# Kernel tuning notes

Measured on AMD Instinct MI355X. Metric: run time of the kernel, lower is better.

## Reference

```python
import jax, jax.numpy as jnp
import numpy as np

B, S, D, H = 4, 2048, 1024, 16
HD = D // H  # head_dim = 64


def setup_inputs() -> dict:
    key = jax.random.key(0)
    ks = jax.random.split(key, 7)
    sc = 0.02
    return {
        "data": jax.random.normal(ks[0], (B, S, D), jnp.float32),
        "context": jax.random.normal(ks[1], (B, S, D), jnp.float32),
        "Wq": jax.random.normal(ks[2], (D, D), jnp.float32) * sc,
        "bq": jnp.zeros((D,), jnp.float32),
        "Wk": jax.random.normal(ks[3], (D, D), jnp.float32) * sc,
        "bk": jnp.zeros((D,), jnp.float32),
        "Wv": jax.random.normal(ks[4], (D, D), jnp.float32) * sc,
        "bv": jnp.zeros((D,), jnp.float32),
        "Wo": jax.random.normal(ks[5], (D, D), jnp.float32) * sc,
        "bo": jnp.zeros((D,), jnp.float32),
    }


def reference(data, context, Wq, bq, Wk, bk, Wv, bv, Wo, bo):
    # Projections (torch Linear: x @ W.T + b; here W stored as [in, out])
    Q = data @ Wq + bq          # [B,S,D]
    K = context @ Wk + bk
    V = context @ Wv + bv
    # split heads -> [B,H,S,HD]
    Q = Q.reshape(B, S, H, HD).transpose(0, 2, 1, 3)
    K = K.reshape(B, S, H, HD).transpose(0, 2, 1, 3)
    V = V.reshape(B, S, H, HD).transpose(0, 2, 1, 3)
    scale = jnp.sqrt(jnp.asarray(HD, Q.dtype))
    scores = jnp.einsum("bhqd,bhkd->bhqk", Q, K) / scale  # [B,H,S,S]
    causal = jnp.tril(jnp.ones((S, S), bool))              # row >= col
    scores = jnp.where(causal[None, None], scores, jnp.asarray(-jnp.inf, scores.dtype))
    probs = jax.nn.softmax(scores, axis=-1)
    Z = jnp.einsum("bhqk,bhkd->bhqd", probs, V)            # [B,H,S,HD]
    Z = Z.transpose(0, 2, 1, 3).reshape(B, S, D)
    return Z @ Wo + bo
```

## Files before the change

kernel.cpp:

```cpp
#include <hip/hip_runtime.h>

#define B_  4
#define S_  2048
#define D_  1024
#define H_  16
#define HD_ 64
#define M_  (B_*S_)

typedef _Float16 f16;
typedef f16  f16x8 __attribute__((ext_vector_type(8)));
typedef f16  f16x4 __attribute__((ext_vector_type(4)));
typedef float f32x4 __attribute__((ext_vector_type(4)));

__device__ __forceinline__ void gload_lds16(const f16* g, f16* l) {
    __builtin_amdgcn_global_load_lds(
        (const __attribute__((address_space(1))) void*)g,
        (__attribute__((address_space(3))) void*)l, 16, 0, 0);
}

__global__ __launch_bounds__(256) void cvt2_kernel(const float* __restrict__ a,
                                                   const float* __restrict__ c,
                                                   f16* __restrict__ out, int n4each) {
    int i = blockIdx.x * 256 + threadIdx.x;
    const float* src = (i < n4each) ? a : c;
    int j = (i < n4each) ? i : i - n4each;
    f32x4 v = *reinterpret_cast<const f32x4*>(src + (size_t)j * 4);
    *reinterpret_cast<f16x4*>(out + (size_t)i * 4) = __builtin_convertvector(v, f16x4);
}

__global__ __launch_bounds__(256) void transpose_cvt4_kernel(const float* __restrict__ Wq,
                                                             const float* __restrict__ Wk,
                                                             const float* __restrict__ Wv,
                                                             const float* __restrict__ Wo,
                                                             f16* __restrict__ WT) {
    __shared__ float tile[32][33];
    const int z = blockIdx.z;
    const float* W = (z == 0) ? Wq : (z == 1) ? Wk : (z == 2) ? Wv : Wo;
    f16* dst = WT + (size_t)z * D_ * D_;
    const int n0 = blockIdx.x * 32, k0 = blockIdx.y * 32;
    const int tx = threadIdx.x & 31, ty = threadIdx.x >> 5;
#pragma unroll
    for (int j = 0; j < 4; ++j)
        tile[ty + 8 * j][tx] = W[(size_t)(k0 + ty + 8 * j) * D_ + n0 + tx];
    __syncthreads();
#pragma unroll
    for (int j = 0; j < 4; ++j)
        dst[(size_t)(n0 + ty + 8 * j) * D_ + k0 + tx] = (f16)tile[tx][ty + 8 * j];
}

__global__ __launch_bounds__(512, 2) void gemm_qkv8(const f16* __restrict__ Adata,
                                                    const f16* __restrict__ Actx,
                                                    const f16* __restrict__ Wt,
                                                    const float* __restrict__ bq,
                                                    const float* __restrict__ bk,
                                                    const float* __restrict__ bv,
                                                    f16* __restrict__ Qb,
                                                    f16* __restrict__ Kb,
                                                    f16* __restrict__ VtB) {
    extern __shared__ __align__(16) f16 SM[];
    constexpr int K = D_;
    constexpr int NT = K / 64;
    const int id = (int)(blockIdx.y * 12 + blockIdx.x);
    const int work = (id & 7) * 48 + (id >> 3);
    const int wy = work / 12, wx = work - wy * 12;
    const int seg = wx >> 2;
    const f16* __restrict__ A = seg ? Actx : Adata;
    const int m0 = wy * 256, n0 = wx * 256;
    const int tid = (int)threadIdx.x;
    const int w = tid >> 6, l = tid & 63, lr = l & 15, lg = l >> 4;
    const int wr = w >> 2, wc = w & 3;
    const int swx = lr & 7;
    const int srow = tid >> 3;
    const int g16 = (tid & 7) ^ (srow & 7);

    auto stageH = [&](int buf, int kt, int mat, int h) {
        const f16* __restrict__ src = mat ? (Wt + (size_t)(n0 + h * 128) * K)
                                          : (A + (size_t)(m0 + h * 128) * K);
        f16* dst = SM + mat * 32768 + buf * 16384 + h * 8192;
        const int kk0 = kt * 64;
        gload_lds16(src + (size_t)srow * K + kk0 + g16 * 8, dst + w * 512);
        gload_lds16(src + (size_t)(srow + 64) * K + kk0 + g16 * 8, dst + 4096 + w * 512);
    };
    auto LDA = [&](int buf, int m, int kk) -> f16x8 {
        const int gr = m * 32 + wr * 16 + lr;
        return *reinterpret_cast<const f16x8*>(
            SM + buf * 16384 + (gr >> 7) * 8192 + (gr & 127) * 64 + (((kk * 4 + lg) ^ swx) * 8));
    };
    auto LDB = [&](int buf, int n, int kk) -> f16x8 {
        const int gr = n * 64 + wc * 16 + lr;
        return *reinterpret_cast<const f16x8*>(
            SM + 32768 + buf * 16384 + (gr >> 7) * 8192 + (gr & 127) * 64 + (((kk * 4 + lg) ^ swx) * 8));
    };

    f32x4 acc[8][4] = {};
    stageH(0, 0, 0, 0); stageH(0, 0, 1, 0); stageH(0, 0, 1, 1); stageH(0, 0, 0, 1);
    asm volatile("s_waitcnt vmcnt(4)" ::: "memory");
    __builtin_amdgcn_s_barrier();

    for (int t = 0; t < NT; ++t) {
        const int buf = t & 1, nb = buf ^ 1;
        const bool nl = (t + 1 < NT);
        f16x8 a[4][2], b[4][2];
#pragma unroll
        for (int m = 0; m < 4; ++m) { a[m][0] = LDA(buf, m, 0); a[m][1] = LDA(buf, m, 1); }
#pragma unroll
        for (int n = 0; n < 2; ++n) { b[n][0] = LDB(buf, n, 0); b[n][1] = LDB(buf, n, 1); }
        if (nl) { stageH(nb, t + 1, 0, 0); asm volatile("s_waitcnt vmcnt(4)" ::: "memory"); }
        else    { asm volatile("s_waitcnt vmcnt(2)" ::: "memory"); }
        __builtin_amdgcn_s_barrier();
        __builtin_amdgcn_s_setprio(1);
#pragma unroll
        for (int kk = 0; kk < 2; ++kk)
#pragma unroll
            for (int m = 0; m < 4; ++m)
#pragma unroll
                for (int n = 0; n < 2; ++n)
                    acc[m][n] = __builtin_amdgcn_mfma_f32_16x16x32_f16(a[m][kk], b[n][kk], acc[m][n], 0, 0, 0);
        __builtin_amdgcn_s_setprio(0);
        __builtin_amdgcn_s_barrier();
#pragma unroll
        for (int n = 2; n < 4; ++n) { b[n][0] = LDB(buf, n, 0); b[n][1] = LDB(buf, n, 1); }
        if (nl) { stageH(nb, t + 1, 1, 0); asm volatile("s_waitcnt vmcnt(4)" ::: "memory"); }
        else    { asm volatile("s_waitcnt vmcnt(0)" ::: "memory"); }
        __builtin_amdgcn_s_barrier();
        __builtin_amdgcn_s_setprio(1);
#pragma unroll
        for (int kk = 0; kk < 2; ++kk)
#pragma unroll
            for (int m = 0; m < 4; ++m)
#pragma unroll
                for (int n = 2; n < 4; ++n)
                    acc[m][n] = __builtin_amdgcn_mfma_f32_16x16x32_f16(a[m][kk], b[n][kk], acc[m][n], 0, 0, 0);
        __builtin_amdgcn_s_setprio(0);
        __builtin_amdgcn_s_barrier();
#pragma unroll
        for (int m = 0; m < 4; ++m) { a[m][0] = LDA(buf, m + 4, 0); a[m][1] = LDA(buf, m + 4, 1); }
        if (nl) stageH(nb, t + 1, 1, 1);
        __builtin_amdgcn_s_barrier();
        __builtin_amdgcn_s_setprio(1);
#pragma unroll
        for (int kk = 0; kk < 2; ++kk)
#pragma unroll
            for (int m = 0; m < 4; ++m)
#pragma unroll
                for (int n = 2; n < 4; ++n)
                    acc[m + 4][n] = __builtin_amdgcn_mfma_f32_16x16x32_f16(a[m][kk], b[n][kk], acc[m + 4][n], 0, 0, 0);
        __builtin_amdgcn_s_setprio(0);
        __builtin_amdgcn_s_barrier();
        if (nl) { stageH(nb, t + 1, 0, 1); asm volatile("s_waitcnt vmcnt(4)" ::: "memory"); }
        __builtin_amdgcn_s_barrier();
        __builtin_amdgcn_s_setprio(1);
#pragma unroll
        for (int kk = 0; kk < 2; ++kk)
#pragma unroll
            for (int m = 0; m < 4; ++m)
#pragma unroll
                for (int n = 0; n < 2; ++n)
                    acc[m + 4][n] = __builtin_amdgcn_mfma_f32_16x16x32_f16(a[m][kk], b[n][kk], acc[m + 4][n], 0, 0, 0);
        __builtin_amdgcn_s_setprio(0);
        __builtin_amdgcn_s_barrier();
    }
    const float* bias = (seg == 0) ? bq : (seg == 1) ? bk : bv;
#pragma unroll
    for (int n = 0; n < 4; ++n) {
        const int col = n0 + n * 64 + wc * 16 + lr;
        const int lc = col & 1023;
        const float bvv = bias[lc];
#pragma unroll
        for (int m = 0; m < 8; ++m) {
            const int row = m0 + m * 32 + wr * 16 + lg * 4;
            if (seg == 2) {
                const int bb = row >> 11, s0 = row & 2047;
                f16x4 v;
#pragma unroll
                for (int r = 0; r < 4; ++r) v[r] = (f16)(acc[m][n][r] + bvv);
                *reinterpret_cast<f16x4*>(VtB + ((size_t)(bb * D_ + lc)) * S_ + s0) = v;
            } else {
                f16* dst = seg ? Kb : Qb;
#pragma unroll
                for (int r = 0; r < 4; ++r)
                    dst[(size_t)(row + r) * D_ + lc] = (f16)(acc[m][n][r] + bvv);
            }
        }
    }
}

__global__ __launch_bounds__(256) void gemm_out(const f16* __restrict__ A,
                                                const f16* __restrict__ Bt,
                                                const float* __restrict__ bias,
                                                float* __restrict__ C) {
    constexpr int K = D_;
    constexpr int NT = K / 32;
    __shared__ __align__(16) f16 Al[2][128 * 32];
    __shared__ __align__(16) f16 Bl[2][128 * 32];
    const int id = (int)(blockIdx.y * 8 + blockIdx.x);
    const int work = (id & 7) * 64 + (id >> 3);
    const int wy = work >> 3, wx = work & 7;
    const int m0 = wy * 128, n0 = wx * 128;
    const int tid = threadIdx.x;
    const int w = tid >> 6, l = tid & 63, lr = l & 15, lg = l >> 4;
    const int wr = w >> 1, wc = w & 1;
    const int srow = tid >> 2, soff = (tid & 3) * 8;

    auto stage = [&](int buf, int kk) {
#pragma unroll
        for (int i = 0; i < 2; ++i) {
            const int row = srow + i * 64;
            gload_lds16(A  + (size_t)(m0 + row) * K + kk + soff, &Al[buf][(w + 4 * i) * 512]);
            gload_lds16(Bt + (size_t)(n0 + row) * K + kk + soff, &Bl[buf][(w + 4 * i) * 512]);
        }
    };

    f32x4 acc[4][4] = {};
    stage(0, 0);
    for (int t = 0; t < NT; ++t) {
        const int buf = t & 1;
        if (t + 1 < NT) {
            stage(buf ^ 1, (t + 1) * 32);
            asm volatile("s_waitcnt vmcnt(4)" ::: "memory");
        } else {
            asm volatile("s_waitcnt vmcnt(0)" ::: "memory");
        }
        __builtin_amdgcn_s_barrier();
        f16x8 a[4], b[4];
#pragma unroll
        for (int m = 0; m < 4; ++m)
            a[m] = *reinterpret_cast<const f16x8*>(&Al[buf][(wr * 64 + m * 16 + lr) * 32 + lg * 8]);
#pragma unroll
        for (int n = 0; n < 4; ++n)
            b[n] = *reinterpret_cast<const f16x8*>(&Bl[buf][(wc * 64 + n * 16 + lr) * 32 + lg * 8]);
        __builtin_amdgcn_s_setprio(1);
#pragma unroll
        for (int m = 0; m < 4; ++m)
#pragma unroll
            for (int n = 0; n < 4; ++n)
                acc[m][n] = __builtin_amdgcn_mfma_f32_16x16x32_f16(a[m], b[n], acc[m][n], 0, 0, 0);
        __builtin_amdgcn_s_setprio(0);
        __builtin_amdgcn_s_barrier();
    }
#pragma unroll
    for (int n = 0; n < 4; ++n) {
        const int col = n0 + wc * 64 + n * 16 + lr;
        const float bv = bias[col];
#pragma unroll
        for (int m = 0; m < 4; ++m) {
            const int row = m0 + wr * 64 + m * 16 + lg * 4;
#pragma unroll
            for (int r = 0; r < 4; ++r)
                C[(size_t)(row + r) * D_ + col] = acc[m][n][r] + bv;
        }
    }
}

__global__ __launch_bounds__(256, 2) void attn_kernel(const f16* __restrict__ Q,
                                                      const f16* __restrict__ Kg,
                                                      const f16* __restrict__ Vt,
                                                      f16* __restrict__ Z) {
    __shared__ __align__(16) f16 KL[2][64 * 64];
    __shared__ __align__(16) f16 VL[2][64 * 64];
    __shared__ __align__(16) f16 Pl[4][32][72];
    const int h = blockIdx.x, b = blockIdx.y, pp = blockIdx.z;
    const int tid = threadIdx.x, w = tid >> 6, l = tid & 63, lr = l & 15, lg = l >> 4;
    const size_t base   = ((size_t)b * S_) * D_ + h * HD_;
    const size_t vtbase = ((size_t)(b * D_ + h * HD_)) * S_;
    const f16* __restrict__ Kbase = Kg + base;
    const f16* __restrict__ Vbase = Vt + vtbase;
    const float sc = 0.125f * 1.44269504f;
    const int sw_xor = lr & 7;

    auto stageKV = [&](int buf, int t0) {
#pragma unroll
        for (int i = 0; i < 2; ++i) {
            const int c = i * 256 + tid;
            const int row = c >> 3, g16 = (c & 7) ^ (row & 7);
            f16* dstK = &KL[buf][(i * 256 + w * 64) * 8];
            f16* dstV = &VL[buf][(i * 256 + w * 64) * 8];
            gload_lds16(Kbase + (size_t)(t0 + row) * D_ + g16 * 8, dstK);
            gload_lds16(Vbase + (size_t)row * S_ + t0 + g16 * 8, dstV);
        }
    };

    for (int half = 0; half < 2; ++half) {
        const int qt = half ? pp : (15 - pp);
        const int q0 = qt * 128, wq0 = q0 + w * 32;
        const int ntw = ((wq0 + 31) >> 6) + 1;
        const int ntb = qt * 2 + 2;

        f16x8 qf[2][2];
#pragma unroll
        for (int mf = 0; mf < 2; ++mf)
#pragma unroll
            for (int kd = 0; kd < 2; ++kd)
                qf[mf][kd] = *reinterpret_cast<const f16x8*>(
                    Q + base + (size_t)(wq0 + mf * 16 + lr) * D_ + kd * 32 + lg * 8);

        f32x4 zacc[2][4] = {};
        float mrun[2] = {-3.0e38f, -3.0e38f}, lsum[2] = {0.f, 0.f};

        stageKV(0, 0);
        for (int t = 0; t < ntb; ++t) {
            const int buf = t & 1;
            if (t + 1 < ntb) {
                stageKV(buf ^ 1, (t + 1) * 64);
                asm volatile("s_waitcnt vmcnt(4)" ::: "memory");
            } else {
                asm volatile("s_waitcnt vmcnt(0)" ::: "memory");
            }
            __builtin_amdgcn_s_barrier();
            if (t < ntw) {
                const int t0 = t * 64;
                f16x8 kf[2][4];
#pragma unroll
                for (int kd = 0; kd < 2; ++kd)
#pragma unroll
                    for (int n = 0; n < 4; ++n)
                        kf[kd][n] = *reinterpret_cast<const f16x8*>(
                            &KL[buf][(n * 16 + lr) * 64 + (((kd * 4 + lg) ^ sw_xor) * 8)]);
                f32x4 sf[2][4] = {};
                __builtin_amdgcn_s_setprio(1);
#pragma unroll
                for (int kd = 0; kd < 2; ++kd)
#pragma unroll
                    for (int n = 0; n < 4; ++n)
#pragma unroll
                        for (int mf = 0; mf < 2; ++mf)
                            sf[mf][n] = __builtin_amdgcn_mfma_f32_16x16x32_f16(kf[kd][n], qf[mf][kd], sf[mf][n], 0, 0, 0);
                __builtin_amdgcn_s_setprio(0);
                f16x8 vf[2][4];
#pragma unroll
                for (int kt = 0; kt < 2; ++kt)
#pragma unroll
                    for (int n = 0; n < 4; ++n)
                        vf[kt][n] = *reinterpret_cast<const f16x8*>(
                            &VL[buf][(n * 16 + lr) * 64 + (((kt * 4 + lg) ^ sw_xor) * 8)]);
                if (t == ntw - 1) {
#pragma unroll
                    for (int mf = 0; mf < 2; ++mf)
#pragma unroll
                        for (int n = 0; n < 4; ++n)
#pragma unroll
                            for (int r = 0; r < 4; ++r)
                                if ((t0 + n * 16 + lg * 4 + r) > (wq0 + mf * 16 + lr))
                                    sf[mf][n][r] = -3.0e38f;
                }
#pragma unroll
                for (int mf = 0; mf < 2; ++mf) {
                    f32x4 t4;
#pragma unroll
                    for (int r = 0; r < 4; ++r)
                        t4[r] = fmaxf(fmaxf(sf[mf][0][r], sf[mf][1][r]), fmaxf(sf[mf][2][r], sf[mf][3][r]));
                    float vmax = fmaxf(fmaxf(t4[0], t4[1]), fmaxf(t4[2], t4[3]));
                    vmax = fmaxf(vmax, __shfl_xor(vmax, 16));
                    vmax = fmaxf(vmax, __shfl_xor(vmax, 32));
                    const float vs = vmax * sc;
                    const bool norm = !__all(vs <= mrun[mf] + 10.0f);
                    float al = 1.0f;
                    if (norm) {
                        const float mnew = fmaxf(mrun[mf], vs);
                        al = __builtin_amdgcn_exp2f(mrun[mf] - mnew);
                        mrun[mf] = mnew;
                    }
                    float s = 0.f;
#pragma unroll
                    for (int n = 0; n < 4; ++n) {
                        f32x4 p;
#pragma unroll
                        for (int r = 0; r < 4; ++r)
                            p[r] = __builtin_amdgcn_exp2f(fmaf(sf[mf][n][r], sc, -mrun[mf]));
                        sf[mf][n] = p;
                        s += (p[0] + p[1]) + (p[2] + p[3]);
                    }
                    s += __shfl_xor(s, 16);
                    s += __shfl_xor(s, 32);
#pragma unroll
                    for (int n = 0; n < 4; ++n) {
                        f16x4 pv;
#pragma unroll
                        for (int r = 0; r < 4; ++r) pv[r] = (f16)sf[mf][n][r];
                        *reinterpret_cast<f16x4*>(&Pl[w][mf * 16 + lr][n * 16 + lg * 4]) = pv;
                    }
                    if (norm) {
                        lsum[mf] = lsum[mf] * al + s;
#pragma unroll
                        for (int r = 0; r < 4; ++r) {
                            const float ar = __shfl(al, lg * 4 + r);
#pragma unroll
                            for (int n = 0; n < 4; ++n) zacc[mf][n][r] *= ar;
                        }
                    } else {
                        lsum[mf] += s;
                    }
                }
#pragma unroll
                for (int kt = 0; kt < 2; ++kt) {
                    f16x8 pa[2];
#pragma unroll
                    for (int mf = 0; mf < 2; ++mf)
                        pa[mf] = *reinterpret_cast<const f16x8*>(&Pl[w][mf * 16 + lr][kt * 32 + lg * 8]);
                    __builtin_amdgcn_s_setprio(1);
#pragma unroll
                    for (int n = 0; n < 4; ++n)
#pragma unroll
                        for (int mf = 0; mf < 2; ++mf)
                            zacc[mf][n] = __builtin_amdgcn_mfma_f32_16x16x32_f16(pa[mf], vf[kt][n], zacc[mf][n], 0, 0, 0);
                    __builtin_amdgcn_s_setprio(0);
                }
            }
            __builtin_amdgcn_s_barrier();
        }
#pragma unroll
        for (int mf = 0; mf < 2; ++mf) {
            const float inv = 1.0f / lsum[mf];
#pragma unroll
            for (int r = 0; r < 4; ++r) {
                const float ir = __shfl(inv, lg * 4 + r);
#pragma unroll
                for (int n = 0; n < 4; ++n)
                    Z[base + (size_t)(wq0 + mf * 16 + lg * 4 + r) * D_ + n * 16 + lr] =
                        (f16)(zacc[mf][n][r] * ir);
            }
        }
    }
}

extern "C" void kernel_launch(void* const* d_in, const int* in_sizes, int n_in,
                              void* d_out, int out_size, void* d_ws, size_t ws_size,
                              hipStream_t stream) {
    const float* data    = (const float*)d_in[0];
    const float* context = (const float*)d_in[1];
    const float* Wq = (const float*)d_in[2];
    const float* bq = (const float*)d_in[3];
    const float* Wk = (const float*)d_in[4];
    const float* bk = (const float*)d_in[5];
    const float* Wv = (const float*)d_in[6];
    const float* bv = (const float*)d_in[7];
    const float* Wo = (const float*)d_in[8];
    const float* bo = (const float*)d_in[9];

    const size_t MD = (size_t)M_ * D_;
    const size_t DD = (size_t)D_ * D_;
    f16* dataB = (f16*)d_ws;
    f16* ctxB  = dataB + MD;
    f16* WqT   = ctxB + MD;
    f16* WkT   = WqT + DD;
    f16* WvT   = WkT + DD;
    f16* WoT   = WvT + DD;
    f16* Qb    = WoT + DD;
    f16* Kb    = Qb + MD;
    f16* VtB   = Kb + MD;
    f16* Zb    = VtB + MD;

    (void)WkT; (void)WvT;

    const int n4 = (int)(MD / 4);
    cvt2_kernel<<<2 * n4 / 256, 256, 0, stream>>>(data, context, dataB, n4);
    transpose_cvt4_kernel<<<dim3(32, 32, 4), 256, 0, stream>>>(Wq, Wk, Wv, Wo, WqT);

    static bool attr_set = false;
    if (!attr_set) {
        hipFuncSetAttribute(reinterpret_cast<const void*>(gemm_qkv8),
                            hipFuncAttributeMaxDynamicSharedMemorySize, 131072);
        attr_set = true;
    }
    gemm_qkv8<<<dim3(12, 32), 512, 131072, stream>>>(dataB, ctxB, WqT, bq, bk, bv, Qb, Kb, VtB);

    attn_kernel<<<dim3(H_, B_, 8), 256, 0, stream>>>(Qb, Kb, VtB, Zb);

    gemm_out<<<dim3(8, 64), 256, 0, stream>>>(Zb, WoT, bo, (float*)d_out);
}
```

Measured before the change: 188.2 us.

## Widen output GEMM tile with triple-buffered swizzled LDS; compute softmax row sums via MFMA

The output projection GEMM now uses 128x256 tiles with a three-stage global-to-LDS pipeline, an XOR-swizzled LDS layout and a single barrier per K step. This halves the block count and raises operand reuse per block. In attention, the per-row softmax denominator is accumulated by an extra MFMA of P against a ones vector instead of shuffle reductions, and rescaling is folded into the norm branch. The row sum now comes from f16-rounded probabilities, which slightly changes numerics. The larger accumulator array adds register pressure, and hipFuncSetAttribute is now called on every launch.

Result: faster. 174.7 us (-7.2%).

```diff
diff --git a/kernel.cpp b/kernel.cpp
--- a/kernel.cpp
+++ b/kernel.cpp
@@ -185,69 +185,93 @@
     }
 }
 
-__global__ __launch_bounds__(256) void gemm_out(const f16* __restrict__ A,
-                                                const f16* __restrict__ Bt,
-                                                const float* __restrict__ bias,
-                                                float* __restrict__ C) {
+__global__ __launch_bounds__(256, 2) void gemm_out3(const f16* __restrict__ A,
+                                                    const f16* __restrict__ Wt,
+                                                    const float* __restrict__ bias,
+                                                    float* __restrict__ Cout) {
+    extern __shared__ __align__(16) f16 SM[];
     constexpr int K = D_;
     constexpr int NT = K / 32;
-    __shared__ __align__(16) f16 Al[2][128 * 32];
-    __shared__ __align__(16) f16 Bl[2][128 * 32];
-    const int id = (int)(blockIdx.y * 8 + blockIdx.x);
-    const int work = (id & 7) * 64 + (id >> 3);
-    const int wy = work >> 3, wx = work & 7;
-    const int m0 = wy * 128, n0 = wx * 128;
-    const int tid = threadIdx.x;
-    const int w = tid >> 6, l = tid & 63, lr = l & 15, lg = l >> 4;
+    const int id = (int)blockIdx.x;
+    const int work = (id & 7) * 32 + (id >> 3);
+    const int wy = work >> 2, wx = work & 3;
+    const int m0 = wy * 128, n0 = wx * 256;
+    const int tid = (int)threadIdx.x;
+    const int w = tid >> 6, lr = tid & 15, lg = (tid & 63) >> 4;
     const int wr = w >> 1, wc = w & 1;
-    const int srow = tid >> 2, soff = (tid & 3) * 8;
-
-    auto stage = [&](int buf, int kk) {
-#pragma unroll
-        for (int i = 0; i < 2; ++i) {
-            const int row = srow + i * 64;
-            gload_lds16(A  + (size_t)(m0 + row) * K + kk + soff, &Al[buf][(w + 4 * i) * 512]);
-            gload_lds16(Bt + (size_t)(n0 + row) * K + kk + soff, &Bl[buf][(w + 4 * i) * 512]);
-        }
-    };
-
-    f32x4 acc[4][4] = {};
+    const int sw = (lr >> 1) & 3;
+
+    auto stage = [&](int buf, int kt) {
+        const int kk0 = kt * 32;
+        f16* base = SM + buf * 12288;
+#pragma unroll
+        for (int j = 0; j < 2; ++j) {
+            const int c = j * 256 + tid;
+            const int row = c >> 2;
+            const int ks = ((c & 3) ^ ((row >> 1) & 3)) * 8;
+            gload_lds16(A + (size_t)(m0 + row) * K + kk0 + ks,
+                        base + (j * 256 + w * 64) * 8);
+        }
+#pragma unroll
+        for (int j = 0; j < 4; ++j) {
+            const int c = j * 256 + tid;
+            const int row = c >> 2;
+            const int ks = ((c & 3) ^ ((row >> 1) & 3)) * 8;
+            gload_lds16(Wt + (size_t)(n0 + row) * K + kk0 + ks,
+                        base + 4096 + (j * 256 + w * 64) * 8);
+        }
+    };
+    auto LDA = [&](int buf, int m) -> f16x8 {
+        return *reinterpret_cast<const f16x8*>(
+            SM + buf * 12288 + (wr * 64 + m * 16 + lr) * 32 + ((lg ^ sw) * 8));
+    };
+    auto LDB = [&](int buf, int n) -> f16x8 {
+        return *reinterpret_cast<const f16x8*>(
+            SM + buf * 12288 + 4096 + (wc * 128 + n * 16 + lr) * 32 + ((lg ^ sw) * 8));
+    };
+
+    f32x4 acc[4][8] = {};
     stage(0, 0);
+    stage(1, 1);
+    asm volatile("s_waitcnt vmcnt(6)" ::: "memory");
+    __builtin_amdgcn_s_barrier();
+
+    int buf = 0;
     for (int t = 0; t < NT; ++t) {
-        const int buf = t & 1;
-        if (t + 1 < NT) {
-            stage(buf ^ 1, (t + 1) * 32);
-            asm volatile("s_waitcnt vmcnt(4)" ::: "memory");
-        } else {
-            asm volatile("s_waitcnt vmcnt(0)" ::: "memory");
-        }
-        __builtin_amdgcn_s_barrier();
-        f16x8 a[4], b[4];
+        if (t + 2 < NT) {
+            int nb = buf + 2; if (nb >= 3) nb -= 3;
+            stage(nb, t + 2);
+        }
+        f16x8 a[4], b[8];
+#pragma unroll
+        for (int m = 0; m < 4; ++m) a[m] = LDA(buf, m);
+#pragma unroll
+        for (int n = 0; n < 8; ++n) b[n] = LDB(buf, n);
+        __builtin_amdgcn_s_setprio(1);
 #pragma unroll
         for (int m = 0; m < 4; ++m)
-            a[m] = *reinterpret_cast<const f16x8*>(&Al[buf][(wr * 64 + m * 16 + lr) * 32 + lg * 8]);
-#pragma unroll
-        for (int n = 0; n < 4; ++n)
-            b[n] = *reinterpret_cast<const f16x8*>(&Bl[buf][(wc * 64 + n * 16 + lr) * 32 + lg * 8]);
-        __builtin_amdgcn_s_setprio(1);
-#pragma unroll
-        for (int m = 0; m < 4; ++m)
-#pragma unroll
-            for (int n = 0; n < 4; ++n)
+#pragma unroll
+            for (int n = 0; n < 8; ++n)
                 acc[m][n] = __builtin_amdgcn_mfma_f32_16x16x32_f16(a[m], b[n], acc[m][n], 0, 0, 0);
         __builtin_amdgcn_s_setprio(0);
-        __builtin_amdgcn_s_barrier();
+        if (t + 2 < NT) {
+            asm volatile("s_waitcnt vmcnt(6)" ::: "memory");
+        } else if (t + 1 < NT) {
+            asm volatile("s_waitcnt vmcnt(0)" ::: "memory");
+        }
+        __builtin_amdgcn_s_barrier();
+        if (++buf >= 3) buf = 0;
     }
 #pragma unroll
-    for (int n = 0; n < 4; ++n) {
-        const int col = n0 + wc * 64 + n * 16 + lr;
-        const float bv = bias[col];
+    for (int n = 0; n < 8; ++n) {
+        const int col = n0 + wc * 128 + n * 16 + lr;
+        const float bvv = bias[col];
 #pragma unroll
         for (int m = 0; m < 4; ++m) {
             const int row = m0 + wr * 64 + m * 16 + lg * 4;
 #pragma unroll
             for (int r = 0; r < 4; ++r)
-                C[(size_t)(row + r) * D_ + col] = acc[m][n][r] + bv;
+                Cout[(size_t)(row + r) * D_ + col] = acc[m][n][r] + bvv;
         }
     }
 }
@@ -267,6 +291,9 @@
     const f16* __restrict__ Vbase = Vt + vtbase;
     const float sc = 0.125f * 1.44269504f;
     const int sw_xor = lr & 7;
+    f16x8 onesv;
+#pragma unroll
+    for (int i = 0; i < 8; ++i) onesv[i] = (f16)1.0f;
 
     auto stageKV = [&](int buf, int t0) {
 #pragma unroll
@@ -295,7 +322,8 @@
                     Q + base + (size_t)(wq0 + mf * 16 + lr) * D_ + kd * 32 + lg * 8);
 
         f32x4 zacc[2][4] = {};
-        float mrun[2] = {-3.0e38f, -3.0e38f}, lsum[2] = {0.f, 0.f};
+        f32x4 lsv[2] = {};
+        float mrun[2] = {-3.0e38f, -3.0e38f};
 
         stageKV(0, 0);
         for (int t = 0; t < ntb; ++t) {
@@ -354,41 +382,28 @@
                     vmax = fmaxf(vmax, __shfl_xor(vmax, 32));
                     const float vs = vmax * sc;
                     const bool norm = !__all(vs <= mrun[mf] + 10.0f);
-                    float al = 1.0f;
                     if (norm) {
                         const float mnew = fmaxf(mrun[mf], vs);
-                        al = __builtin_amdgcn_exp2f(mrun[mf] - mnew);
+                        const float al = __builtin_amdgcn_exp2f(mrun[mf] - mnew);
                         mrun[mf] = mnew;
+#pragma unroll
+                        for (int r = 0; r < 4; ++r) {
+                            const float ar = __shfl(al, lg * 4 + r);
+#pragma unroll
+                            for (int n = 0; n < 4; ++n) zacc[mf][n][r] *= ar;
+                            lsv[mf][r] *= ar;
+                        }
                     }
-                    float s = 0.f;
 #pragma unroll
                     for (int n = 0; n < 4; ++n) {
                         f32x4 p;
 #pragma unroll
                         for (int r = 0; r < 4; ++r)
                             p[r] = __builtin_amdgcn_exp2f(fmaf(sf[mf][n][r], sc, -mrun[mf]));
-                        sf[mf][n] = p;
-                        s += (p[0] + p[1]) + (p[2] + p[3]);
-                    }
-                    s += __shfl_xor(s, 16);
-                    s += __shfl_xor(s, 32);
-#pragma unroll
-                    for (int n = 0; n < 4; ++n) {
                         f16x4 pv;
 #pragma unroll
-                        for (int r = 0; r < 4; ++r) pv[r] = (f16)sf[mf][n][r];
+                        for (int r = 0; r < 4; ++r) pv[r] = (f16)p[r];
                         *reinterpret_cast<f16x4*>(&Pl[w][mf * 16 + lr][n * 16 + lg * 4]) = pv;
-                    }
-                    if (norm) {
-                        lsum[mf] = lsum[mf] * al + s;
-#pragma unroll
-                        for (int r = 0; r < 4; ++r) {
-                            const float ar = __shfl(al, lg * 4 + r);
-#pragma unroll
-                            for (int n = 0; n < 4; ++n) zacc[mf][n][r] *= ar;
-                        }
-                    } else {
-                        lsum[mf] += s;
                     }
                 }
 #pragma unroll
@@ -403,6 +418,9 @@
 #pragma unroll
                         for (int mf = 0; mf < 2; ++mf)
                             zacc[mf][n] = __builtin_amdgcn_mfma_f32_16x16x32_f16(pa[mf], vf[kt][n], zacc[mf][n], 0, 0, 0);
+#pragma unroll
+                    for (int mf = 0; mf < 2; ++mf)
+                        lsv[mf] = __builtin_amdgcn_mfma_f32_16x16x32_f16(pa[mf], onesv, lsv[mf], 0, 0, 0);
                     __builtin_amdgcn_s_setprio(0);
                 }
             }
@@ -410,15 +428,15 @@
         }
 #pragma unroll
         for (int mf = 0; mf < 2; ++mf) {
-            const float inv = 1.0f / lsum[mf];
-#pragma unroll
-            for (int r = 0; r < 4; ++r) {
-                const float ir = __shfl(inv, lg * 4 + r);
+            f32x4 inv;
+#pragma unroll
+            for (int r = 0; r < 4; ++r) inv[r] = 1.0f / lsv[mf][r];
+#pragma unroll
+            for (int r = 0; r < 4; ++r)
 #pragma unroll
                 for (int n = 0; n < 4; ++n)
                     Z[base + (size_t)(wq0 + mf * 16 + lg * 4 + r) * D_ + n * 16 + lr] =
-                        (f16)(zacc[mf][n][r] * ir);
-            }
+                        (f16)(zacc[mf][n][r] * inv[r]);
         }
     }
 }
@@ -456,15 +474,15 @@
     cvt2_kernel<<<2 * n4 / 256, 256, 0, stream>>>(data, context, dataB, n4);
     transpose_cvt4_kernel<<<dim3(32, 32, 4), 256, 0, stream>>>(Wq, Wk, Wv, Wo, WqT);
 
-    static bool attr_set = false;
-    if (!attr_set) {
-        hipFuncSetAttribute(reinterpret_cast<const void*>(gemm_qkv8),
-                            hipFuncAttributeMaxDynamicSharedMemorySize, 131072);
-        attr_set = true;
-    }
-    gemm_qkv8<<<dim3(12, 32), 512, 131072, stream>>>(dataB, ctxB, WqT, bq, bk, bv, Qb, Kb, VtB);
+    hipFuncSetAttribute(reinterpret_cast<const void*>(gemm_qkv8),
+                        hipFuncAttributeMaxDynamicSharedMemorySize, 131072);
+    hipFuncSetAttribute(reinterpret_cast<const void*>(gemm_out3),
+                        hipFuncAttributeMaxDynamicSharedMemorySize, 73728);
+
+    gemm_qkv8<<<dim3(12, 32), 512, 131072, stream>>>(dataB, ctxB, WqT, bq, bk, bv,
+                                                     Qb, Kb, VtB);
 
     attn_kernel<<<dim3(H_, B_, 8), 256, 0, stream>>>(Qb, Kb, VtB, Zb);
 
-    gemm_out<<<dim3(8, 64), 256, 0, stream>>>(Zb, WoT, bo, (float*)d_out);
-}
+    gemm_out3<<<256, 256, 73728, stream>>>(Zb, WoT, bo, (float*)d_out);
+}
```
